# Kernel tuning notes

Hardware: AMD Instinct MI355X
Metric: run time of the kernel (lower is better)

Reference implementation:

```python
import jax, jax.numpy as jnp
import numpy as np

VOCAB, EMB, HID, LABELS = 50000, 300, 200, 10
B, S = 32, 512


def _gru_direction(emb, h0, w_ih, w_hh, b_ih, b_hh):
    """Run a GRUCell recurrence over time. emb: [B,S,E], h0: [B,H] -> [B,S,H].
    PyTorch GRUCell gate order: r, z, n."""
    # Precompute input projections for all timesteps (one big GEMM).
    gi = jnp.einsum('bse,ge->bsg', emb, w_ih) + b_ih  # [B,S,3H]
    gi = jnp.transpose(gi, (1, 0, 2))  # [S,B,3H] for scan
    H = h0.shape[-1]

    def step(h, gi_t):
        gh = h @ w_hh.T + b_hh  # [B,3H]
        i_r, i_z, i_n = gi_t[:, :H], gi_t[:, H:2 * H], gi_t[:, 2 * H:]
        h_r, h_z, h_n = gh[:, :H], gh[:, H:2 * H], gh[:, 2 * H:]
        r = jax.nn.sigmoid(i_r + h_r)
        z = jax.nn.sigmoid(i_z + h_z)
        n = jnp.tanh(i_n + r * h_n)
        h_new = (1.0 - z) * n + z * h
        return h_new, h_new

    _, hs = jax.lax.scan(step, h0, gi)  # hs: [S,B,H]
    return jnp.transpose(hs, (1, 0, 2))  # [B,S,H]


def setup_inputs() -> dict:
    key = jax.random.key(0)
    ks = jax.random.split(key, 14)
    sc = 0.05
    return {
        'text': jax.random.randint(ks[0], (B, S), 0, VOCAB),
        'embedding': jax.random.normal(ks[1], (VOCAB, EMB), jnp.float32) * sc,
        'w_ih_f': jax.random.normal(ks[2], (3 * HID, EMB), jnp.float32) * sc,
        'w_hh_f': jax.random.normal(ks[3], (3 * HID, HID), jnp.float32) * sc,
        'b_ih_f': jax.random.normal(ks[4], (3 * HID,), jnp.float32) * sc,
        'b_hh_f': jax.random.normal(ks[5], (3 * HID,), jnp.float32) * sc,
        'w_ih_b': jax.random.normal(ks[6], (3 * HID, EMB), jnp.float32) * sc,
        'w_hh_b': jax.random.normal(ks[7], (3 * HID, HID), jnp.float32) * sc,
        'b_ih_b': jax.random.normal(ks[8], (3 * HID,), jnp.float32) * sc,
        'b_hh_b': jax.random.normal(ks[9], (3 * HID,), jnp.float32) * sc,
        'lin_w': jax.random.normal(ks[10], (LABELS, 2 * HID), jnp.float32) * sc,
        'lin_b': jax.random.normal(ks[11], (LABELS,), jnp.float32) * sc,
        'h0_f': jax.random.uniform(ks[12], (B, HID), jnp.float32),
        'h0_b': jax.random.uniform(ks[13], (B, HID), jnp.float32),
    }


def reference(text, embedding, w_ih_f, w_hh_f, b_ih_f, b_hh_f,
              w_ih_b, w_hh_b, b_ih_b, b_hh_b, lin_w, lin_b, h0_f, h0_b):
    emb = embedding[text]  # [B,S,E]
    hid = w_hh_f.shape[-1]
    h0f = (h0_f - 0.5) / hid  # matches (rand-0.5)/hidden_unit
    h0b = (h0_b - 0.5) / hid
    out_f = _gru_direction(emb, h0f, w_ih_f, w_hh_f, b_ih_f, b_hh_f)
    # backward direction: iterate t = S-1 .. 0, outputs re-ordered to time order
    out_b = _gru_direction(emb[:, ::-1, :], h0b, w_ih_b, w_hh_b, b_ih_b, b_hh_b)[:, ::-1, :]
    out = jnp.concatenate([out_f, out_b], axis=2)  # [B,S,2H]
    preds = out @ lin_w.T + lin_b  # [B,S,LABELS]
    return preds
```

## Files before the change

kernel.cpp:

```cpp
#include <hip/hip_runtime.h>
#include <hip/hip_fp16.h>

typedef _Float16 h8 __attribute__((ext_vector_type(8)));
typedef _Float16 h4 __attribute__((ext_vector_type(4)));
typedef _Float16 h2 __attribute__((ext_vector_type(2)));
typedef float f4 __attribute__((ext_vector_type(4)));

#define EMB    300
#define HID    200
#define NR     600
#define KP     320
#define NPAD   1216
#define SEQ    512
#define MTOT   16384

#if defined(__has_builtin)
#if __has_builtin(__builtin_amdgcn_fdot2)
#define USE_FDOT2 1
#endif
#endif

__device__ __forceinline__ float fdot2f(h2 a, h2 b, float c) {
#ifdef USE_FDOT2
  return __builtin_amdgcn_fdot2(a, b, c, false);
#else
  return c + (float)a[0] * (float)b[0] + (float)a[1] * (float)b[1];
#endif
}

__device__ __forceinline__ float sigm(float x) { return 1.0f / (1.0f + __expf(-x)); }
__device__ __forceinline__ float tanhf_(float x) { return 1.0f - 2.0f / (1.0f + __expf(2.0f * x)); }

__global__ __launch_bounds__(256) void prep_kernel(
    const float* __restrict__ w_ih_f, const float* __restrict__ w_ih_b,
    const float* __restrict__ b_ih_f, const float* __restrict__ b_ih_b,
    _Float16* __restrict__ Wcvt, float* __restrict__ bias_cat) {
  int idx = blockIdx.x * 256 + threadIdx.x;
  if (idx < NPAD * KP) {
    int n = idx / KP, k = idx - n * KP;
    float v = 0.0f;
    if (k < EMB) {
      if (n < NR) v = w_ih_f[n * EMB + k];
      else if (n < 2 * NR) v = w_ih_b[(n - NR) * EMB + k];
    }
    Wcvt[idx] = (_Float16)v;
  }
  if (idx < NPAD) {
    float bv = 0.0f;
    if (idx < NR) bv = b_ih_f[idx];
    else if (idx < 2 * NR) bv = b_ih_b[idx - NR];
    bias_cat[idx] = bv;
  }
}

__global__ __launch_bounds__(512) void gi_gemm(
    const int* __restrict__ text, const float* __restrict__ emb,
    const _Float16* __restrict__ Wcvt, const float* __restrict__ bias_cat,
    __half* __restrict__ gi) {
  __shared__ _Float16 At[128][328];
  const int t = threadIdx.x;
  const int m0 = blockIdx.x * 128;
  {
    const int row = t >> 2;
    const int q = t & 3;
    const int tokid = text[m0 + row];
    const float4* ep = (const float4*)(emb + (size_t)tokid * EMB);
    for (int c4 = q; c4 < 75; c4 += 4) {
      float4 v = ep[c4];
      h4 hv = { (_Float16)v.x, (_Float16)v.y, (_Float16)v.z, (_Float16)v.w };
      *(h4*)&At[row][c4 * 4] = hv;
    }
    for (int c = 300 + q; c < 328; c += 4) At[row][c] = (_Float16)0.0f;
  }
  __syncthreads();

  const int wv = t >> 6, lane = t & 63;
  const int l15 = lane & 15, l4 = lane >> 4;
  const int nhalf = wv >> 2;
  const int ms0 = (wv & 3) * 2;
  const int r0 = ms0 * 16 + l15;
  const int r1 = r0 + 16;

  for (int c2 = 0; c2 < 2; ++c2) {
    const int nbase = nhalf * 38 + c2 * 19;
    f4 acc0[19], acc1[19];
#pragma unroll
    for (int i = 0; i < 19; ++i) { acc0[i] = (f4){0,0,0,0}; acc1[i] = (f4){0,0,0,0}; }
    for (int ks = 0; ks < 10; ++ks) {
      h8 a0 = *(const h8*)&At[r0][ks * 32 + l4 * 8];
      h8 a1 = *(const h8*)&At[r1][ks * 32 + l4 * 8];
#pragma unroll
      for (int i = 0; i < 19; ++i) {
        const h8* bp = (const h8*)(Wcvt + (size_t)((nbase + i) * 16 + l15) * KP + ks * 32 + l4 * 8);
        h8 bf = *bp;
        acc0[i] = __builtin_amdgcn_mfma_f32_16x16x32_f16(a0, bf, acc0[i], 0, 0, 0);
        acc1[i] = __builtin_amdgcn_mfma_f32_16x16x32_f16(a1, bf, acc1[i], 0, 0, 0);
      }
    }
#pragma unroll
    for (int i = 0; i < 19; ++i) {
      const int n = (nbase + i) * 16 + l15;
      const float bv = bias_cat[n];
#pragma unroll
      for (int j = 0; j < 4; ++j) {
        const int mA = m0 + ms0 * 16 + l4 * 4 + j;
        gi[(size_t)mA * NPAD + n] = (__half)(acc0[i][j] + bv);
        gi[(size_t)(mA + 16) * NPAD + n] = (__half)(acc1[i][j] + bv);
      }
    }
  }
}

__global__ __launch_bounds__(512, 2) void gru_rec(
    const float* __restrict__ w_hh_f, const float* __restrict__ b_hh_f,
    const float* __restrict__ w_hh_b, const float* __restrict__ b_hh_b,
    const float* __restrict__ h0_f,  const float* __restrict__ h0_b,
    const __half* __restrict__ gi, __half* __restrict__ hs) {
  const int t = threadIdx.x;
  const int dir = blockIdx.x >> 5;
  const int b = blockIdx.x & 31;
  const float* w_hh = dir ? w_hh_b : w_hh_f;
  const float* bhh_g = dir ? b_hh_b : b_hh_f;
  const float* h0 = dir ? h0_b : h0_f;

  __shared__ __align__(16) _Float16 h_pad[4 * 64];
  __shared__ float h_f[HID];
  __shared__ float y_lds[NR];
  __shared__ float bhh[NR];
  __shared__ __align__(16) _Float16 gi_lds[2][NR + 8];

  const int rg = t >> 2, kg = t & 3;

  h2 wpk[5][25];
#pragma unroll
  for (int i = 0; i < 5; ++i) {
    const int r = rg * 5 + i;
    const bool valid = (r < NR);
    const float* wr = w_hh + (size_t)(valid ? r : 0) * HID + kg * 50;
#pragma unroll
    for (int kk = 0; kk < 25; ++kk) {
      float w0 = valid ? wr[2 * kk] : 0.0f;
      float w1 = valid ? wr[2 * kk + 1] : 0.0f;
      wpk[i][kk] = (h2){ (_Float16)w0, (_Float16)w1 };
    }
  }

  for (int j = t; j < HID; j += 512) {
    float hv = (h0[b * HID + j] - 0.5f) * (1.0f / (float)HID);
    h_f[j] = hv;
    int p = j >> 1;
    h_pad[(p / 25) * 64 + (p % 25) * 2 + (j & 1)] = (_Float16)hv;
  }
  for (int j = t; j < NR; j += 512) bhh[j] = bhh_g[j];
  {
    const int s0 = dir ? (SEQ - 1) : 0;
    const h2* g0 = (const h2*)(gi + (size_t)(b * SEQ + s0) * NPAD + dir * NR);
    if (t < NR / 2) ((h2*)gi_lds[0])[t] = g0[t];
  }
  __syncthreads();

  const h2* hb = (const h2*)&h_pad[kg * 64];

  for (int st = 0; st < SEQ; ++st) {
    const int s = dir ? (SEQ - 1 - st) : st;
    h2 pf = (h2){(_Float16)0.0f, (_Float16)0.0f};
    const bool do_pf = (t < NR / 2) && (st < SEQ - 1);
    if (do_pf) {
      const int sn = dir ? (SEQ - 2 - st) : (st + 1);
      const h2* gn = (const h2*)(gi + (size_t)(b * SEQ + sn) * NPAD + dir * NR);
      pf = gn[t];
    }
    h2 hp[25];
#pragma unroll
    for (int kk = 0; kk < 25; ++kk) hp[kk] = hb[kk];
    float a0 = 0, a1 = 0, a2 = 0, a3 = 0, a4 = 0;
#pragma unroll
    for (int kk = 0; kk < 25; ++kk) {
      a0 = fdot2f(wpk[0][kk], hp[kk], a0);
      a1 = fdot2f(wpk[1][kk], hp[kk], a1);
      a2 = fdot2f(wpk[2][kk], hp[kk], a2);
      a3 = fdot2f(wpk[3][kk], hp[kk], a3);
      a4 = fdot2f(wpk[4][kk], hp[kk], a4);
    }
    a0 += __shfl_xor(a0, 1); a0 += __shfl_xor(a0, 2);
    a1 += __shfl_xor(a1, 1); a1 += __shfl_xor(a1, 2);
    a2 += __shfl_xor(a2, 1); a2 += __shfl_xor(a2, 2);
    a3 += __shfl_xor(a3, 1); a3 += __shfl_xor(a3, 2);
    a4 += __shfl_xor(a4, 1); a4 += __shfl_xor(a4, 2);
    if (kg == 0 && rg < 120) {
      const int r = rg * 5;
      y_lds[r] = a0; y_lds[r + 1] = a1; y_lds[r + 2] = a2;
      y_lds[r + 3] = a3; y_lds[r + 4] = a4;
    }
    __syncthreads();
    if (t < HID) {
      const _Float16* gih = gi_lds[st & 1];
      const float ir = (float)gih[t];
      const float iz = (float)gih[HID + t];
      const float inn = (float)gih[2 * HID + t];
      const float yr = y_lds[t] + bhh[t];
      const float yz = y_lds[HID + t] + bhh[HID + t];
      const float yn = y_lds[2 * HID + t] + bhh[2 * HID + t];
      const float r = sigm(ir + yr);
      const float z = sigm(iz + yz);
      const float n = tanhf_(inn + r * yn);
      const float hnew = (1.0f - z) * n + z * h_f[t];
      h_f[t] = hnew;
      const int p = t >> 1;
      h_pad[(p / 25) * 64 + (p % 25) * 2 + (t & 1)] = (_Float16)hnew;
      hs[(size_t)(b * SEQ + s) * 400 + dir * HID + t] = (__half)hnew;
    }
    if (do_pf) ((h2*)gi_lds[(st + 1) & 1])[t] = pf;
    __syncthreads();
  }
}

__global__ __launch_bounds__(256) void final_linear(
    const __half* __restrict__ hs, const float* __restrict__ lin_w,
    const float* __restrict__ lin_b, float* __restrict__ out) {
  __shared__ _Float16 hsl[64][400];
  __shared__ _Float16 lwl[10][400];
  const int t = threadIdx.x;
  const int m0 = blockIdx.x * 64;
  const ushort4* hp = (const ushort4*)(hs + (size_t)m0 * 400);
  for (int idx = t; idx < 64 * 100; idx += 256) {
    ushort4 v = hp[idx];
    const int row = idx / 100, c = idx - row * 100;
    *(ushort4*)&hsl[row][c * 4] = v;
  }
  for (int idx = t; idx < 10 * 400; idx += 256) {
    (&lwl[0][0])[idx] = (_Float16)lin_w[idx];
  }
  __syncthreads();
  for (int idx = t; idx < 640; idx += 256) {
    const int m = idx / 10, c = idx - (idx / 10) * 10;
    const h2* hr = (const h2*)hsl[m];
    const h2* wr = (const h2*)lwl[c];
    float acc = 0.0f;
#pragma unroll 8
    for (int kk = 0; kk < 200; ++kk) acc = fdot2f(hr[kk], wr[kk], acc);
    out[(size_t)(m0 + m) * 10 + c] = acc + lin_b[c];
  }
}

extern "C" void kernel_launch(void* const* d_in, const int* in_sizes, int n_in,
                              void* d_out, int out_size, void* d_ws, size_t ws_size,
                              hipStream_t stream) {
  const int*   text   = (const int*)d_in[0];
  const float* emb    = (const float*)d_in[1];
  const float* w_ih_f = (const float*)d_in[2];
  const float* w_hh_f = (const float*)d_in[3];
  const float* b_ih_f = (const float*)d_in[4];
  const float* b_hh_f = (const float*)d_in[5];
  const float* w_ih_b = (const float*)d_in[6];
  const float* w_hh_b = (const float*)d_in[7];
  const float* b_ih_b = (const float*)d_in[8];
  const float* b_hh_b = (const float*)d_in[9];
  const float* lin_w  = (const float*)d_in[10];
  const float* lin_b  = (const float*)d_in[11];
  const float* h0_f   = (const float*)d_in[12];
  const float* h0_b   = (const float*)d_in[13];
  float* out = (float*)d_out;

  char* ws = (char*)d_ws;
  _Float16* Wcvt     = (_Float16*)(ws);
  float*    bias_cat = (float*)(ws + 778240);
  __half*   gi       = (__half*)(ws + 783360);
  __half*   hs       = (__half*)(ws + 40629248);

  prep_kernel<<<dim3((NPAD * KP + 255) / 256), dim3(256), 0, stream>>>(
      w_ih_f, w_ih_b, b_ih_f, b_ih_b, Wcvt, bias_cat);
  gi_gemm<<<dim3(MTOT / 128), dim3(512), 0, stream>>>(
      text, emb, Wcvt, bias_cat, gi);
  gru_rec<<<dim3(64), dim3(512), 0, stream>>>(
      w_hh_f, b_hh_f, w_hh_b, b_hh_b, h0_f, h0_b, gi, hs);
  final_linear<<<dim3(MTOT / 64), dim3(256), 0, stream>>>(
      hs, lin_w, lin_b, out);
}
```

Before: 893.1 us.

## Restructure GRU recurrence so each thread owns one hidden unit's three gate rows

The recurrent kernel now uses 256 threads per block. Each active thread holds all 300 h2 weights for its hidden unit's r, z and n rows in registers and computes the full 200-length dot products itself. This removes the 4-way k-split with its shuffle reductions, the y_lds staging and one of the two barriers per timestep, and it keeps the hidden state in a register with a double-buffered h_pad. The weights are pre-packed into a coalesced fp16 pair layout by prep_kernel, and gi prefetch uses 8-byte loads. The cost is heavy register pressure, around 300 VGPRs for the weights, which risks spills, and each step now runs a serial chain of 100 dot2 operations per thread.

```diff
diff --git a/kernel.cpp b/kernel.cpp
--- a/kernel.cpp
+++ b/kernel.cpp
@@ -34,7 +34,9 @@
 __global__ __launch_bounds__(256) void prep_kernel(
     const float* __restrict__ w_ih_f, const float* __restrict__ w_ih_b,
     const float* __restrict__ b_ih_f, const float* __restrict__ b_ih_b,
-    _Float16* __restrict__ Wcvt, float* __restrict__ bias_cat) {
+    const float* __restrict__ w_hh_f, const float* __restrict__ w_hh_b,
+    _Float16* __restrict__ Wcvt, float* __restrict__ bias_cat,
+    h2* __restrict__ Whh2) {
   int idx = blockIdx.x * 256 + threadIdx.x;
   if (idx < NPAD * KP) {
     int n = idx / KP, k = idx - n * KP;
@@ -50,6 +52,15 @@
     if (idx < NR) bv = b_ih_f[idx];
     else if (idx < 2 * NR) bv = b_ih_b[idx - NR];
     bias_cat[idx] = bv;
+  }
+  if (idx < 2 * 100 * NR) {
+    int d = idx / (100 * NR);
+    int rem = idx - d * (100 * NR);
+    int kk = rem / NR, r = rem - kk * NR;
+    const float* w = d ? w_hh_b : w_hh_f;
+    float w0 = w[r * HID + 2 * kk];
+    float w1 = w[r * HID + 2 * kk + 1];
+    Whh2[idx] = (h2){ (_Float16)w0, (_Float16)w1 };
   }
 }
 
@@ -111,106 +122,82 @@
   }
 }
 
-__global__ __launch_bounds__(512, 2) void gru_rec(
-    const float* __restrict__ w_hh_f, const float* __restrict__ b_hh_f,
-    const float* __restrict__ w_hh_b, const float* __restrict__ b_hh_b,
+__global__ __launch_bounds__(256, 1) void gru_rec(
+    const h2* __restrict__ Whh2,
+    const float* __restrict__ b_hh_f, const float* __restrict__ b_hh_b,
     const float* __restrict__ h0_f,  const float* __restrict__ h0_b,
     const __half* __restrict__ gi, __half* __restrict__ hs) {
   const int t = threadIdx.x;
   const int dir = blockIdx.x >> 5;
   const int b = blockIdx.x & 31;
-  const float* w_hh = dir ? w_hh_b : w_hh_f;
   const float* bhh_g = dir ? b_hh_b : b_hh_f;
   const float* h0 = dir ? h0_b : h0_f;
 
-  __shared__ __align__(16) _Float16 h_pad[4 * 64];
-  __shared__ float h_f[HID];
-  __shared__ float y_lds[NR];
-  __shared__ float bhh[NR];
-  __shared__ __align__(16) _Float16 gi_lds[2][NR + 8];
-
-  const int rg = t >> 2, kg = t & 3;
-
-  h2 wpk[5][25];
-#pragma unroll
-  for (int i = 0; i < 5; ++i) {
-    const int r = rg * 5 + i;
-    const bool valid = (r < NR);
-    const float* wr = w_hh + (size_t)(valid ? r : 0) * HID + kg * 50;
-#pragma unroll
-    for (int kk = 0; kk < 25; ++kk) {
-      float w0 = valid ? wr[2 * kk] : 0.0f;
-      float w1 = valid ? wr[2 * kk + 1] : 0.0f;
-      wpk[i][kk] = (h2){ (_Float16)w0, (_Float16)w1 };
-    }
-  }
-
-  for (int j = t; j < HID; j += 512) {
-    float hv = (h0[b * HID + j] - 0.5f) * (1.0f / (float)HID);
-    h_f[j] = hv;
-    int p = j >> 1;
-    h_pad[(p / 25) * 64 + (p % 25) * 2 + (j & 1)] = (_Float16)hv;
-  }
-  for (int j = t; j < NR; j += 512) bhh[j] = bhh_g[j];
+  __shared__ __align__(16) _Float16 h_pad[2][208];
+  __shared__ __align__(16) _Float16 gi_lds[2][608];
+
+  const int u = t;
+  const bool act = (u < HID);
+  const int us = act ? u : 0;
+
+  h2 w0[100], w1[100], w2[100];
+  const h2* Wd = Whh2 + (size_t)dir * 100 * NR;
+#pragma unroll
+  for (int kk = 0; kk < 100; ++kk) {
+    w0[kk] = Wd[kk * NR + us];
+    w1[kk] = Wd[kk * NR + 200 + us];
+    w2[kk] = Wd[kk * NR + 400 + us];
+  }
+  float b0 = 0, b1 = 0, b2 = 0, hreg = 0;
+  if (act) {
+    b0 = bhh_g[u]; b1 = bhh_g[200 + u]; b2 = bhh_g[400 + u];
+    hreg = (h0[b * HID + u] - 0.5f) * (1.0f / (float)HID);
+    h_pad[0][u] = (_Float16)hreg;
+  }
   {
     const int s0 = dir ? (SEQ - 1) : 0;
-    const h2* g0 = (const h2*)(gi + (size_t)(b * SEQ + s0) * NPAD + dir * NR);
-    if (t < NR / 2) ((h2*)gi_lds[0])[t] = g0[t];
+    const h4* g0 = (const h4*)(gi + (size_t)(b * SEQ + s0) * NPAD + dir * NR);
+    if (t < 150) ((h4*)gi_lds[0])[t] = g0[t];
   }
   __syncthreads();
 
-  const h2* hb = (const h2*)&h_pad[kg * 64];
-
   for (int st = 0; st < SEQ; ++st) {
+    const int cur = st & 1, nxt = cur ^ 1;
     const int s = dir ? (SEQ - 1 - st) : st;
-    h2 pf = (h2){(_Float16)0.0f, (_Float16)0.0f};
-    const bool do_pf = (t < NR / 2) && (st < SEQ - 1);
+    h4 pf = (h4){(_Float16)0, (_Float16)0, (_Float16)0, (_Float16)0};
+    const bool do_pf = (t < 150) && (st < SEQ - 1);
     if (do_pf) {
       const int sn = dir ? (SEQ - 2 - st) : (st + 1);
-      const h2* gn = (const h2*)(gi + (size_t)(b * SEQ + sn) * NPAD + dir * NR);
-      pf = gn[t];
-    }
-    h2 hp[25];
-#pragma unroll
-    for (int kk = 0; kk < 25; ++kk) hp[kk] = hb[kk];
-    float a0 = 0, a1 = 0, a2 = 0, a3 = 0, a4 = 0;
-#pragma unroll
-    for (int kk = 0; kk < 25; ++kk) {
-      a0 = fdot2f(wpk[0][kk], hp[kk], a0);
-      a1 = fdot2f(wpk[1][kk], hp[kk], a1);
-      a2 = fdot2f(wpk[2][kk], hp[kk], a2);
-      a3 = fdot2f(wpk[3][kk], hp[kk], a3);
-      a4 = fdot2f(wpk[4][kk], hp[kk], a4);
-    }
-    a0 += __shfl_xor(a0, 1); a0 += __shfl_xor(a0, 2);
-    a1 += __shfl_xor(a1, 1); a1 += __shfl_xor(a1, 2);
-    a2 += __shfl_xor(a2, 1); a2 += __shfl_xor(a2, 2);
-    a3 += __shfl_xor(a3, 1); a3 += __shfl_xor(a3, 2);
-    a4 += __shfl_xor(a4, 1); a4 += __shfl_xor(a4, 2);
-    if (kg == 0 && rg < 120) {
-      const int r = rg * 5;
-      y_lds[r] = a0; y_lds[r + 1] = a1; y_lds[r + 2] = a2;
-      y_lds[r + 3] = a3; y_lds[r + 4] = a4;
-    }
-    __syncthreads();
-    if (t < HID) {
-      const _Float16* gih = gi_lds[st & 1];
-      const float ir = (float)gih[t];
-      const float iz = (float)gih[HID + t];
-      const float inn = (float)gih[2 * HID + t];
-      const float yr = y_lds[t] + bhh[t];
-      const float yz = y_lds[HID + t] + bhh[HID + t];
-      const float yn = y_lds[2 * HID + t] + bhh[2 * HID + t];
+      pf = ((const h4*)(gi + (size_t)(b * SEQ + sn) * NPAD + dir * NR))[t];
+    }
+    float a0a = 0, a0b = 0, a1a = 0, a1b = 0, a2a = 0, a2b = 0;
+#pragma unroll
+    for (int c = 0; c < 25; ++c) {
+      h8 hv = *(const h8*)&h_pad[cur][c * 8];
+      h2 p0 = {hv[0], hv[1]}, p1 = {hv[2], hv[3]};
+      h2 p2 = {hv[4], hv[5]}, p3 = {hv[6], hv[7]};
+      a0a = fdot2f(w0[c * 4 + 0], p0, a0a); a0b = fdot2f(w0[c * 4 + 1], p1, a0b);
+      a0a = fdot2f(w0[c * 4 + 2], p2, a0a); a0b = fdot2f(w0[c * 4 + 3], p3, a0b);
+      a1a = fdot2f(w1[c * 4 + 0], p0, a1a); a1b = fdot2f(w1[c * 4 + 1], p1, a1b);
+      a1a = fdot2f(w1[c * 4 + 2], p2, a1a); a1b = fdot2f(w1[c * 4 + 3], p3, a1b);
+      a2a = fdot2f(w2[c * 4 + 0], p0, a2a); a2b = fdot2f(w2[c * 4 + 1], p1, a2b);
+      a2a = fdot2f(w2[c * 4 + 2], p2, a2a); a2b = fdot2f(w2[c * 4 + 3], p3, a2b);
+    }
+    if (act) {
+      const float yr = a0a + a0b + b0;
+      const float yz = a1a + a1b + b1;
+      const float yn = a2a + a2b + b2;
+      const float ir = (float)gi_lds[cur][u];
+      const float iz = (float)gi_lds[cur][200 + u];
+      const float inn = (float)gi_lds[cur][400 + u];
       const float r = sigm(ir + yr);
       const float z = sigm(iz + yz);
       const float n = tanhf_(inn + r * yn);
-      const float hnew = (1.0f - z) * n + z * h_f[t];
-      h_f[t] = hnew;
-      const int p = t >> 1;
-      h_pad[(p / 25) * 64 + (p % 25) * 2 + (t & 1)] = (_Float16)hnew;
-      hs[(size_t)(b * SEQ + s) * 400 + dir * HID + t] = (__half)hnew;
-    }
-    if (do_pf) ((h2*)gi_lds[(st + 1) & 1])[t] = pf;
+      hreg = (1.0f - z) * n + z * hreg;
+      h_pad[nxt][u] = (_Float16)hreg;
+      hs[(size_t)(b * SEQ + s) * 400 + dir * HID + u] = (__half)hreg;
+    }
+    if (do_pf) ((h4*)gi_lds[nxt])[t] = pf;
     __syncthreads();
   }
 }
@@ -267,13 +254,14 @@
   float*    bias_cat = (float*)(ws + 778240);
   __half*   gi       = (__half*)(ws + 783360);
   __half*   hs       = (__half*)(ws + 40629248);
+  h2*       Whh2     = (h2*)(ws + 53736448);
 
   prep_kernel<<<dim3((NPAD * KP + 255) / 256), dim3(256), 0, stream>>>(
-      w_ih_f, w_ih_b, b_ih_f, b_ih_b, Wcvt, bias_cat);
+      w_ih_f, w_ih_b, b_ih_f, b_ih_b, w_hh_f, w_hh_b, Wcvt, bias_cat, Whh2);
   gi_gemm<<<dim3(MTOT / 128), dim3(512), 0, stream>>>(
       text, emb, Wcvt, bias_cat, gi);
-  gru_rec<<<dim3(64), dim3(512), 0, stream>>>(
-      w_hh_f, b_hh_f, w_hh_b, b_hh_b, h0_f, h0_b, gi, hs);
+  gru_rec<<<dim3(64), dim3(256), 0, stream>>>(
+      Whh2, b_hh_f, b_hh_b, h0_f, h0_b, gi, hs);
   final_linear<<<dim3(MTOT / 64), dim3(256), 0, stream>>>(
       hs, lin_w, lin_b, out);
 }
```

Result: slower. 1.238 ms (+38.6%).
